# Optimization experiments

Hardware: AMD Instinct MI355X
Metric: run time of the kernel (lower is better)

## Reference

```python
import jax, jax.numpy as jnp
import numpy as np

SOS_TOKEN = 1
B, H, V, T = 64, 1024, 32000, 40
INPUT_SIZE = 4096


def setup_inputs() -> dict:
    key = jax.random.key(0)
    ks = jax.random.split(key, 12)
    s = 1.0 / np.sqrt(H)
    return {
        "output": jax.random.normal(ks[0], (B, INPUT_SIZE), jnp.float32),
        "h0": jax.random.normal(ks[1], (1, B, H), jnp.float32),
        "c0": jax.random.normal(ks[2], (1, B, H), jnp.float32),
        "target_outputs": jax.random.randint(ks[3], (B, T), 0, V, jnp.int64),
        "target_lengths": jnp.full((B,), T, jnp.int64),
        "embed": jax.random.normal(ks[4], (V, H), jnp.float32),
        "w_ih": jax.random.uniform(ks[5], (4 * H, H), jnp.float32, -s, s),
        "w_hh": jax.random.uniform(ks[6], (4 * H, H), jnp.float32, -s, s),
        "b_ih": jax.random.uniform(ks[7], (4 * H,), jnp.float32, -s, s),
        "b_hh": jax.random.uniform(ks[8], (4 * H,), jnp.float32, -s, s),
        "w_out": jax.random.uniform(ks[9], (V, H), jnp.float32, -s, s),
        "b_out": jax.random.uniform(ks[10], (V,), jnp.float32, -s, s),
    }


def _lstm_cell(x, h, c, w_ih, w_hh, b_ih, b_hh):
    # PyTorch LSTMCell math; gate order i, f, g, o
    gates = x @ w_ih.T + b_ih + h @ w_hh.T + b_hh  # [B, 4H]
    i, f, g, o = jnp.split(gates, 4, axis=-1)
    c2 = jax.nn.sigmoid(f) * c + jax.nn.sigmoid(i) * jnp.tanh(g)
    h2 = jax.nn.sigmoid(o) * jnp.tanh(c2)
    return h2, c2


def reference(output, h0, c0, target_outputs, target_lengths,
              embed, w_ih, w_hh, b_ih, b_hh, w_out, b_out):
    batch = output.shape[0]
    max_lens = int(jnp.max(target_lengths))
    h, c = h0[0], c0[0]  # num_layers=1 -> [B, H]

    # Initial symbol = SOS; initial dec_o = W(embed(SOS)) (no LSTM), as in torch code
    symbol0 = jnp.full((batch,), SOS_TOKEN, dtype=target_outputs.dtype)
    dec_o0 = embed[symbol0] @ w_out.T + b_out  # [B, V]

    def step(carry, _):
        symbol, dec_o, h, c = carry
        # emit current (symbol, dec_o), then decode next
        x = embed[symbol]  # [B, H]
        h2, c2 = _lstm_cell(x, h, c, w_ih, w_hh, b_ih, b_hh)
        dec2 = h2 @ w_out.T + b_out  # [B, V]
        sym2 = jnp.argmax(dec2, axis=-1).astype(symbol.dtype)  # greedy topk(1)
        return (sym2, dec2, h2, c2), (symbol, dec_o)
    (_, _, _, _), (symbols, decs) = jax.lax.scan(
        step, (symbol0, dec_o0, h, c), None, length=max_lens)

    decoder_outs = jnp.transpose(decs, (1, 0, 2))  # [B, T, V]
    symbol_outs = jnp.transpose(symbols, (1, 0))   # [B, T]
    return decoder_outs, symbol_outs
```

## Files before the change

kernel.cpp:

```cpp
#include <hip/hip_runtime.h>

#define Bdim 64
#define Hdim 1024
#define Vdim 32000
#define Tdim 40

typedef __bf16 bf16x8 __attribute__((ext_vector_type(8)));
typedef float  f32x4  __attribute__((ext_vector_type(4)));
static_assert(sizeof(bf16x8) == 16, "bf16x8 must be 16B");

__device__ __forceinline__ unsigned long long pack_key(float f, int v) {
    unsigned u = __float_as_uint(f);
    u = (u & 0x80000000u) ? ~u : (u | 0x80000000u);
    return ((unsigned long long)u << 32) | (unsigned long long)(0xFFFFFFFFu - (unsigned)v);
}

__device__ __forceinline__ void gll16(const void* g, void* l) {
    __builtin_amdgcn_global_load_lds(
        (const __attribute__((address_space(1))) void*)g,
        (__attribute__((address_space(3))) void*)l, 16, 0, 0);
}

__device__ __forceinline__ void bsplit3(float x, unsigned short& a, unsigned short& b,
                                        unsigned short& c) {
    __bf16 h = (__bf16)x;  float r  = x - (float)h;
    __bf16 m = (__bf16)r;  float r2 = r - (float)m;
    __bf16 l = (__bf16)r2;
    a = __builtin_bit_cast(unsigned short, h);
    b = __builtin_bit_cast(unsigned short, m);
    c = __builtin_bit_cast(unsigned short, l);
}

template<int NCH, bool ARGMAX, bool BIAS>
__device__ __forceinline__ void mm_core(
    const float* __restrict__ W,
    const unsigned short* __restrict__ Ah,
    const unsigned short* __restrict__ Am,
    const unsigned short* __restrict__ Al,
    int n0, const float* __restrict__ bias,
    float* __restrict__ out, size_t out_bstride,
    unsigned long long* __restrict__ slots)
{
    __shared__ __align__(16) unsigned char smem[2][20480];
    __shared__ unsigned long long red[4][4][16];

    const int tid  = threadIdx.x;
    const int lane = tid & 63;
    const int wid  = tid >> 6;

    f32x4 acc[4] = {};

    const unsigned char* Wb = (const unsigned char*)W;
    const unsigned char* Apb[3] = {(const unsigned char*)Ah, (const unsigned char*)Am,
                                   (const unsigned char*)Al};

    const int arws = tid >> 2, acs = tid & 3;
    const size_t asrc_off = (size_t)arws * 4096 + (size_t)(acs ^ ((arws >> 1) & 3)) * 16;

    auto stage = [&](int bufidx, int ch) {
        unsigned char* bb = smem[bufidx];
        const size_t kb4 = (size_t)ch * 128;
        const size_t kb2 = (size_t)ch * 64;
#pragma unroll
        for (int s = 0; s < 2; s++) {
            int gg = tid + 256 * s;
            int rw = gg >> 3, cc = gg & 7;
            int sg = cc ^ (rw & 7);
            gll16(Wb + (size_t)rw * 4096 + kb4 + (size_t)sg * 16,
                  bb + ((wid * 64 + 256 * s) << 4));
        }
#pragma unroll
        for (int pl = 0; pl < 3; pl++)
            gll16(Apb[pl] + asrc_off + kb2, bb + 8192 + pl * 4096 + (wid << 10));
    };

    stage(0, 0);
    __syncthreads();

    const int col  = lane & 15;
    const int kg   = lane >> 4;
    const int wrow = wid * 16 + col;
    const int wg0  = (2 * kg) ^ (wrow & 7);
    const int wg1  = (2 * kg + 1) ^ (wrow & 7);

#pragma unroll 2
    for (int ch = 0; ch < NCH; ch++) {
        if (ch + 1 < NCH) stage((ch + 1) & 1, ch + 1);
        unsigned char* base = smem[ch & 1];

        const unsigned char* Wr = base + wrow * 128;
        f32x4 w0 = *(const f32x4*)(Wr + (wg0 << 4));
        f32x4 w1 = *(const f32x4*)(Wr + (wg1 << 4));
        bf16x8 whi, wmid, wlo;
#pragma unroll
        for (int j = 0; j < 4; j++) {
            float x0 = w0[j], x1 = w1[j];
            __bf16 a0 = (__bf16)x0; float r0 = x0 - (float)a0;
            __bf16 b0 = (__bf16)r0; float q0 = r0 - (float)b0;
            whi[j] = a0; wmid[j] = b0; wlo[j] = (__bf16)q0;
            __bf16 a1 = (__bf16)x1; float r1 = x1 - (float)a1;
            __bf16 b1 = (__bf16)r1; float q1 = r1 - (float)b1;
            whi[4 + j] = a1; wmid[4 + j] = b1; wlo[4 + j] = (__bf16)q1;
        }
#pragma unroll
        for (int bt = 0; bt < 4; bt++) {
            const int arow = bt * 16 + col;
            const unsigned char* Ar = base + 8192 + arow * 64
                                    + ((kg ^ ((arow >> 1) & 3)) << 4);
            bf16x8 ahi = *(const bf16x8*)Ar;
            bf16x8 ami = *(const bf16x8*)(Ar + 4096);
            bf16x8 alo = *(const bf16x8*)(Ar + 8192);
            acc[bt] = __builtin_amdgcn_mfma_f32_16x16x32_bf16(whi,  ahi, acc[bt], 0, 0, 0);
            acc[bt] = __builtin_amdgcn_mfma_f32_16x16x32_bf16(whi,  ami, acc[bt], 0, 0, 0);
            acc[bt] = __builtin_amdgcn_mfma_f32_16x16x32_bf16(wmid, ahi, acc[bt], 0, 0, 0);
            acc[bt] = __builtin_amdgcn_mfma_f32_16x16x32_bf16(whi,  alo, acc[bt], 0, 0, 0);
            acc[bt] = __builtin_amdgcn_mfma_f32_16x16x32_bf16(wlo,  ahi, acc[bt], 0, 0, 0);
            acc[bt] = __builtin_amdgcn_mfma_f32_16x16x32_bf16(wmid, ami, acc[bt], 0, 0, 0);
        }
        __syncthreads();
    }

    const int ncol = n0 + wid * 16 + kg * 4;
    f32x4 bv = {};
    if (BIAS) bv = *(const f32x4*)(bias + ncol);

    unsigned long long bk[4];
#pragma unroll
    for (int bt = 0; bt < 4; bt++) {
        const int b = bt * 16 + col;
        float* op = out + (size_t)b * out_bstride + ncol;
        f32x4 vv;
        unsigned long long best = 0ull;
#pragma unroll
        for (int r = 0; r < 4; r++) {
            float val = acc[bt][r];
            if (BIAS) val += bv[r];
            vv[r] = val;
            if (ARGMAX) {
                unsigned long long key = pack_key(val, ncol + r);
                if (key > best) best = key;
            }
        }
        *(f32x4*)op = vv;
        bk[bt] = best;
    }

    if (ARGMAX) {
#pragma unroll
        for (int bt = 0; bt < 4; bt++) {
            unsigned long long k = bk[bt];
            unsigned long long o = __shfl_xor(k, 16, 64); if (o > k) k = o;
            o = __shfl_xor(k, 32, 64);                    if (o > k) k = o;
            if (lane < 16) red[wid][bt][lane] = k;
        }
        __syncthreads();
        if (tid < 64) {
            const int bt = tid >> 4, c = tid & 15;
            unsigned long long k = red[0][bt][c];
            if (red[1][bt][c] > k) k = red[1][bt][c];
            if (red[2][bt][c] > k) k = red[2][bt][c];
            if (red[3][bt][c] > k) k = red[3][bt][c];
            atomicMax(&slots[bt * 16 + c], k);
        }
    }
}

template<bool AM>
__global__ __launch_bounds__(256, 2) void k_logits(
    const float* __restrict__ w_out,
    const unsigned short* __restrict__ ah, const unsigned short* __restrict__ am,
    const unsigned short* __restrict__ al,
    const float* __restrict__ b_out, float* __restrict__ out,
    unsigned long long* __restrict__ slots)
{
    const int vb = blockIdx.x * 64;
    mm_core<32, AM, true>(w_out + (size_t)vb * Hdim, ah, am, al, vb, b_out,
                          out, (size_t)Tdim * Vdim, slots);
}

__global__ __launch_bounds__(256, 2) void k_gates(
    const float* __restrict__ w_ih, const float* __restrict__ w_hh,
    const unsigned short* __restrict__ xh_hi, const unsigned short* __restrict__ xh_mid,
    const unsigned short* __restrict__ xh_lo, float* __restrict__ gp)
{
    const int nb = blockIdx.x * 64;
    const int y = blockIdx.y, z = blockIdx.z;
    const float* W = (y ? w_hh : w_ih) + (size_t)nb * Hdim + z * 256;
    const int ao = y * 1024 + z * 256;
    mm_core<8, false, false>(W, xh_hi + ao, xh_mid + ao, xh_lo + ao, nb, nullptr,
                             gp + (size_t)(y * 4 + z) * (Bdim * 4096), 4096, nullptr);
}

__global__ void k_cell(const float* __restrict__ gp, const float* __restrict__ b_ih,
                       const float* __restrict__ b_hh, float* __restrict__ cbuf,
                       unsigned short* __restrict__ xh_hi, unsigned short* __restrict__ xh_mid,
                       unsigned short* __restrict__ xh_lo,
                       unsigned long long* __restrict__ slots)
{
    const int idx = blockIdx.x * 256 + threadIdx.x;
    const int b = idx >> 10, k = idx & 1023;
    const size_t S = (size_t)Bdim * 4096;
    const size_t base = (size_t)b * 4096;
    float g[4];
#pragma unroll
    for (int q = 0; q < 4; q++) {
        size_t o = base + q * 1024 + k;
        float s = gp[o];
#pragma unroll
        for (int i = 1; i < 8; i++) s += gp[i * S + o];
        g[q] = s + b_ih[q * 1024 + k] + b_hh[q * 1024 + k];
    }
    float si = 1.f / (1.f + expf(-g[0]));
    float sf = 1.f / (1.f + expf(-g[1]));
    float so = 1.f / (1.f + expf(-g[3]));
    float c  = cbuf[idx];
    float c2 = sf * c + si * tanhf(g[2]);
    float h2 = so * tanhf(c2);
    cbuf[idx] = c2;
    const size_t o = (size_t)b * 2048 + 1024 + k;
    unsigned short hs, ms, ls;
    bsplit3(h2, hs, ms, ls);
    xh_hi[o] = hs; xh_mid[o] = ms; xh_lo[o] = ls;
    if (idx < 64) slots[idx] = 0ull;
}

__global__ void k_symgather(const unsigned long long* __restrict__ slots,
                            const float* __restrict__ embed,
                            unsigned short* __restrict__ xh_hi,
                            unsigned short* __restrict__ xh_mid,
                            unsigned short* __restrict__ xh_lo,
                            float* __restrict__ sym_out, int t)
{
    __shared__ int s_sym;
    const int b = blockIdx.x, tid = threadIdx.x;
    if (tid == 0) {
        unsigned long long key = slots[b];
        int v = (int)(0xFFFFFFFFu - (unsigned)(key & 0xFFFFFFFFull));
        s_sym = v;
        sym_out[b * Tdim + t] = (float)v;
    }
    __syncthreads();
    const int v = s_sym;
    float4 e = *(const float4*)(embed + (size_t)v * Hdim + tid * 4);
    ushort4 hi, mi, lo;
    bsplit3(e.x, hi.x, mi.x, lo.x);
    bsplit3(e.y, hi.y, mi.y, lo.y);
    bsplit3(e.z, hi.z, mi.z, lo.z);
    bsplit3(e.w, hi.w, mi.w, lo.w);
    const size_t o = (size_t)b * 2048 + tid * 4;
    *(ushort4*)(xh_hi + o) = hi;
    *(ushort4*)(xh_mid + o) = mi;
    *(ushort4*)(xh_lo + o) = lo;
}

__global__ void k_init(const float* __restrict__ embed, const float* __restrict__ h0,
                       const float* __restrict__ c0,
                       unsigned short* __restrict__ xh_hi, unsigned short* __restrict__ xh_mid,
                       unsigned short* __restrict__ xh_lo,
                       float* __restrict__ cbuf, float* __restrict__ sym_out)
{
    const int b = blockIdx.x, tid = threadIdx.x;
    if (tid == 0) sym_out[b * Tdim] = 1.0f;
    const size_t xo = (size_t)b * 2048 + tid * 4;
    ushort4 hi, mi, lo;

    float4 e = *(const float4*)(embed + Hdim + tid * 4);
    bsplit3(e.x, hi.x, mi.x, lo.x);
    bsplit3(e.y, hi.y, mi.y, lo.y);
    bsplit3(e.z, hi.z, mi.z, lo.z);
    bsplit3(e.w, hi.w, mi.w, lo.w);
    *(ushort4*)(xh_hi + xo) = hi; *(ushort4*)(xh_mid + xo) = mi; *(ushort4*)(xh_lo + xo) = lo;

    float4 h = *(const float4*)(h0 + (size_t)b * Hdim + tid * 4);
    bsplit3(h.x, hi.x, mi.x, lo.x);
    bsplit3(h.y, hi.y, mi.y, lo.y);
    bsplit3(h.z, hi.z, mi.z, lo.z);
    bsplit3(h.w, hi.w, mi.w, lo.w);
    *(ushort4*)(xh_hi + xo + 1024) = hi;
    *(ushort4*)(xh_mid + xo + 1024) = mi;
    *(ushort4*)(xh_lo + xo + 1024) = lo;

    float4 c = *(const float4*)(c0 + (size_t)b * Hdim + tid * 4);
    *(float4*)(cbuf + (size_t)b * Hdim + tid * 4) = c;
}

extern "C" void kernel_launch(void* const* d_in, const int* in_sizes, int n_in,
                              void* d_out, int out_size, void* d_ws, size_t ws_size,
                              hipStream_t stream)
{
    const float* h0    = (const float*)d_in[1];
    const float* c0    = (const float*)d_in[2];
    const float* embed = (const float*)d_in[5];
    const float* w_ih  = (const float*)d_in[6];
    const float* w_hh  = (const float*)d_in[7];
    const float* b_ih  = (const float*)d_in[8];
    const float* b_hh  = (const float*)d_in[9];
    const float* w_out = (const float*)d_in[10];
    const float* b_out = (const float*)d_in[11];

    float* out = (float*)d_out;
    float* sym_out = out + (size_t)Bdim * Tdim * Vdim;

    unsigned short* xh_hi  = (unsigned short*)d_ws;
    unsigned short* xh_mid = xh_hi + (size_t)Bdim * 2048;
    unsigned short* xh_lo  = xh_mid + (size_t)Bdim * 2048;
    float* cbuf = (float*)(xh_lo + (size_t)Bdim * 2048);
    float* gp   = cbuf + (size_t)Bdim * Hdim;
    unsigned long long* slots = (unsigned long long*)(gp + 8ull * Bdim * 4096);

    k_init<<<Bdim, 256, 0, stream>>>(embed, h0, c0, xh_hi, xh_mid, xh_lo, cbuf, sym_out);

    k_logits<false><<<Vdim / 64, 256, 0, stream>>>(w_out, xh_hi, xh_mid, xh_lo,
                                                   b_out, out, slots);

    for (int t = 0; t < Tdim - 1; t++) {
        k_gates<<<dim3(64, 2, 4), 256, 0, stream>>>(w_ih, w_hh, xh_hi, xh_mid, xh_lo, gp);
        k_cell<<<Bdim * Hdim / 256, 256, 0, stream>>>(gp, b_ih, b_hh, cbuf,
                                                      xh_hi, xh_mid, xh_lo, slots);
        k_logits<true><<<Vdim / 64, 256, 0, stream>>>(w_out,
                                                      xh_hi + 1024, xh_mid + 1024, xh_lo + 1024,
                                                      b_out, out + (size_t)(t + 1) * Vdim, slots);
        k_symgather<<<Bdim, 256, 0, stream>>>(slots, embed, xh_hi, xh_mid, xh_lo,
                                              sym_out, t + 1);
    }
}
```

Baseline: 2.714 ms.

## Fuse symbol gather into gates GEMM and widen logits blocks to 128 columns

Removes the separate symbol-gather kernel: the x-half of the gates GEMM now decodes the argmax slot, gathers the embedding row directly from global memory and splits it into bf16 planes while staging into LDS. The logits kernel is widened to 8 waves covering 128 vocab columns per block (250 blocks, 512 threads), so the shared activation tiles are loaded once for twice as many output columns. The workspace is split into separate h and x planes, and a final tiny kernel writes the last symbol. This saves one launch per step and some A-tile traffic, but the gather path performs synchronous loads and conversion inside the pipelined stage, and the larger logits blocks change occupancy.

```diff
diff --git a/kernel.cpp b/kernel.cpp
--- a/kernel.cpp
+++ b/kernel.cpp
@@ -7,6 +7,7 @@
 
 typedef __bf16 bf16x8 __attribute__((ext_vector_type(8)));
 typedef float  f32x4  __attribute__((ext_vector_type(4)));
+typedef unsigned short u16x8 __attribute__((ext_vector_type(8)));
 static_assert(sizeof(bf16x8) == 16, "bf16x8 must be 16B");
 
 __device__ __forceinline__ unsigned long long pack_key(float f, int v) {
@@ -15,34 +16,53 @@
     return ((unsigned long long)u << 32) | (unsigned long long)(0xFFFFFFFFu - (unsigned)v);
 }
 
+__device__ __forceinline__ int decode_key(unsigned long long key) {
+    return (int)(0xFFFFFFFFu - (unsigned)(key & 0xFFFFFFFFull));
+}
+
 __device__ __forceinline__ void gll16(const void* g, void* l) {
     __builtin_amdgcn_global_load_lds(
         (const __attribute__((address_space(1))) void*)g,
         (__attribute__((address_space(3))) void*)l, 16, 0, 0);
 }
 
-__device__ __forceinline__ void bsplit3(float x, unsigned short& a, unsigned short& b,
-                                        unsigned short& c) {
+struct BSplit { unsigned short h, m, l; };
+
+__device__ __forceinline__ BSplit bsplit3v(float x) {
     __bf16 h = (__bf16)x;  float r  = x - (float)h;
     __bf16 m = (__bf16)r;  float r2 = r - (float)m;
     __bf16 l = (__bf16)r2;
-    a = __builtin_bit_cast(unsigned short, h);
-    b = __builtin_bit_cast(unsigned short, m);
-    c = __builtin_bit_cast(unsigned short, l);
-}
-
-template<int NCH, bool ARGMAX, bool BIAS>
+    BSplit s;
+    s.h = __builtin_bit_cast(unsigned short, h);
+    s.m = __builtin_bit_cast(unsigned short, m);
+    s.l = __builtin_bit_cast(unsigned short, l);
+    return s;
+}
+
+__device__ __forceinline__ void bsplit3(float x, unsigned short& a, unsigned short& b,
+                                        unsigned short& c) {
+    BSplit s = bsplit3v(x);
+    a = s.h; b = s.m; c = s.l;
+}
+
+template<int NW, int NCH, bool ARGMAX, bool BIAS, bool GATHER>
 __device__ __forceinline__ void mm_core(
+    unsigned char* sm,
+    unsigned long long (*red)[4][16],
     const float* __restrict__ W,
     const unsigned short* __restrict__ Ah,
     const unsigned short* __restrict__ Am,
     const unsigned short* __restrict__ Al,
+    const float* __restrict__ Gsrc,
+    const unsigned long long* __restrict__ slots_in, int tstep,
+    float* __restrict__ sym_dst,
     int n0, const float* __restrict__ bias,
     float* __restrict__ out, size_t out_bstride,
-    unsigned long long* __restrict__ slots)
-{
-    __shared__ __align__(16) unsigned char smem[2][20480];
-    __shared__ unsigned long long red[4][4][16];
+    unsigned long long* __restrict__ slots_out)
+{
+    constexpr int NT     = NW * 64;
+    constexpr int WBYTES = NW * 2048;
+    constexpr int BUFSZ  = WBYTES + 12288;
 
     const int tid  = threadIdx.x;
     const int lane = tid & 63;
@@ -54,24 +74,63 @@
     const unsigned char* Apb[3] = {(const unsigned char*)Ah, (const unsigned char*)Am,
                                    (const unsigned char*)Al};
 
-    const int arws = tid >> 2, acs = tid & 3;
-    const size_t asrc_off = (size_t)arws * 4096 + (size_t)(acs ^ ((arws >> 1) & 3)) * 16;
+    const int ar = tid >> 2, as = tid & 3;
+    const int aswz = as ^ ((ar >> 1) & 3);
+    const size_t asrc_off = (size_t)ar * 2048 + (size_t)aswz * 16;
+    const size_t aldst    = (size_t)ar * 64 + (size_t)aswz * 16;
+
+    const float* grow = nullptr;
+    if constexpr (GATHER) {
+        if (tid < 256) {
+            int symv = 1;
+            if (tstep > 0) {
+                unsigned long long key = slots_in[ar];
+                symv = decode_key(key);
+                if (sym_dst != nullptr && as == 0)
+                    sym_dst[ar * Tdim + tstep] = (float)symv;
+            }
+            grow = Gsrc + (size_t)symv * 1024 + as * 8;
+        }
+    }
 
     auto stage = [&](int bufidx, int ch) {
-        unsigned char* bb = smem[bufidx];
+        unsigned char* bb = sm + bufidx * BUFSZ;
         const size_t kb4 = (size_t)ch * 128;
-        const size_t kb2 = (size_t)ch * 64;
 #pragma unroll
         for (int s = 0; s < 2; s++) {
-            int gg = tid + 256 * s;
+            int gg = tid + NT * s;
             int rw = gg >> 3, cc = gg & 7;
             int sg = cc ^ (rw & 7);
             gll16(Wb + (size_t)rw * 4096 + kb4 + (size_t)sg * 16,
-                  bb + ((wid * 64 + 256 * s) << 4));
-        }
-#pragma unroll
-        for (int pl = 0; pl < 3; pl++)
-            gll16(Apb[pl] + asrc_off + kb2, bb + 8192 + pl * 4096 + (wid << 10));
+                  bb + ((wid * 64 + NT * s) << 4));
+        }
+        if constexpr (GATHER) {
+            if (tid < 256) {
+                const float* p = grow + ch * 32;
+                float4 f0 = *(const float4*)(p);
+                float4 f1 = *(const float4*)(p + 4);
+                u16x8 vh, vm, vl;
+                BSplit s0 = bsplit3v(f0.x); vh[0] = s0.h; vm[0] = s0.m; vl[0] = s0.l;
+                BSplit s1 = bsplit3v(f0.y); vh[1] = s1.h; vm[1] = s1.m; vl[1] = s1.l;
+                BSplit s2 = bsplit3v(f0.z); vh[2] = s2.h; vm[2] = s2.m; vl[2] = s2.l;
+                BSplit s3 = bsplit3v(f0.w); vh[3] = s3.h; vm[3] = s3.m; vl[3] = s3.l;
+                BSplit s4 = bsplit3v(f1.x); vh[4] = s4.h; vm[4] = s4.m; vl[4] = s4.l;
+                BSplit s5 = bsplit3v(f1.y); vh[5] = s5.h; vm[5] = s5.m; vl[5] = s5.l;
+                BSplit s6 = bsplit3v(f1.z); vh[6] = s6.h; vm[6] = s6.m; vl[6] = s6.l;
+                BSplit s7 = bsplit3v(f1.w); vh[7] = s7.h; vm[7] = s7.m; vl[7] = s7.l;
+                *(u16x8*)(bb + WBYTES + aldst)        = vh;
+                *(u16x8*)(bb + WBYTES + 4096 + aldst) = vm;
+                *(u16x8*)(bb + WBYTES + 8192 + aldst) = vl;
+            }
+        } else {
+            if (tid < 256) {
+                const size_t kb2 = (size_t)ch * 64;
+#pragma unroll
+                for (int pl = 0; pl < 3; pl++)
+                    gll16(Apb[pl] + asrc_off + kb2,
+                          bb + WBYTES + pl * 4096 + (wid << 10));
+            }
+        }
     };
 
     stage(0, 0);
@@ -86,7 +145,7 @@
 #pragma unroll 2
     for (int ch = 0; ch < NCH; ch++) {
         if (ch + 1 < NCH) stage((ch + 1) & 1, ch + 1);
-        unsigned char* base = smem[ch & 1];
+        unsigned char* base = sm + (ch & 1) * BUFSZ;
 
         const unsigned char* Wr = base + wrow * 128;
         f32x4 w0 = *(const f32x4*)(Wr + (wg0 << 4));
@@ -105,7 +164,7 @@
 #pragma unroll
         for (int bt = 0; bt < 4; bt++) {
             const int arow = bt * 16 + col;
-            const unsigned char* Ar = base + 8192 + arow * 64
+            const unsigned char* Ar = base + WBYTES + arow * 64
                                     + ((kg ^ ((arow >> 1) & 3)) << 4);
             bf16x8 ahi = *(const bf16x8*)Ar;
             bf16x8 ami = *(const bf16x8*)(Ar + 4096);
@@ -145,7 +204,7 @@
         bk[bt] = best;
     }
 
-    if (ARGMAX) {
+    if constexpr (ARGMAX) {
 #pragma unroll
         for (int bt = 0; bt < 4; bt++) {
             unsigned long long k = bk[bt];
@@ -157,44 +216,56 @@
         if (tid < 64) {
             const int bt = tid >> 4, c = tid & 15;
             unsigned long long k = red[0][bt][c];
-            if (red[1][bt][c] > k) k = red[1][bt][c];
-            if (red[2][bt][c] > k) k = red[2][bt][c];
-            if (red[3][bt][c] > k) k = red[3][bt][c];
-            atomicMax(&slots[bt * 16 + c], k);
+#pragma unroll
+            for (int w = 1; w < NW; w++)
+                if (red[w][bt][c] > k) k = red[w][bt][c];
+            atomicMax(&slots_out[bt * 16 + c], k);
         }
     }
 }
 
 template<bool AM>
-__global__ __launch_bounds__(256, 2) void k_logits(
+__global__ __launch_bounds__(512, 1) void k_logits(
     const float* __restrict__ w_out,
     const unsigned short* __restrict__ ah, const unsigned short* __restrict__ am,
     const unsigned short* __restrict__ al,
     const float* __restrict__ b_out, float* __restrict__ out,
     unsigned long long* __restrict__ slots)
 {
-    const int vb = blockIdx.x * 64;
-    mm_core<32, AM, true>(w_out + (size_t)vb * Hdim, ah, am, al, vb, b_out,
-                          out, (size_t)Tdim * Vdim, slots);
+    __shared__ __align__(16) unsigned char smem[2][28672];
+    __shared__ unsigned long long red[8][4][16];
+    const int vb = blockIdx.x * 128;
+    mm_core<8, 32, AM, true, false>(&smem[0][0], red,
+        w_out + (size_t)vb * Hdim, ah, am, al, nullptr, nullptr, 0, nullptr,
+        vb, b_out, out, (size_t)Tdim * Vdim, slots);
 }
 
 __global__ __launch_bounds__(256, 2) void k_gates(
     const float* __restrict__ w_ih, const float* __restrict__ w_hh,
-    const unsigned short* __restrict__ xh_hi, const unsigned short* __restrict__ xh_mid,
-    const unsigned short* __restrict__ xh_lo, float* __restrict__ gp)
-{
-    const int nb = blockIdx.x * 64;
-    const int y = blockIdx.y, z = blockIdx.z;
-    const float* W = (y ? w_hh : w_ih) + (size_t)nb * Hdim + z * 256;
-    const int ao = y * 1024 + z * 256;
-    mm_core<8, false, false>(W, xh_hi + ao, xh_mid + ao, xh_lo + ao, nb, nullptr,
-                             gp + (size_t)(y * 4 + z) * (Bdim * 4096), 4096, nullptr);
+    const unsigned short* __restrict__ hh, const unsigned short* __restrict__ hm,
+    const unsigned short* __restrict__ hl,
+    const float* __restrict__ embed, unsigned long long* __restrict__ slots,
+    int t, float* __restrict__ sym_out, float* __restrict__ gp)
+{
+    __shared__ __align__(16) unsigned char smem[2][20480];
+    const int nbi = blockIdx.x, y = blockIdx.y, z = blockIdx.z;
+    const float* W = (y ? w_hh : w_ih) + (size_t)nbi * 65536 + z * 256;
+    float* gout = gp + (size_t)(y * 4 + z) * (Bdim * 4096);
+    if (y)
+        mm_core<4, 8, false, false, false>(&smem[0][0], nullptr, W,
+            hh + z * 256, hm + z * 256, hl + z * 256, nullptr, nullptr, t, nullptr,
+            nbi * 64, nullptr, gout, 4096, nullptr);
+    else
+        mm_core<4, 8, false, false, true>(&smem[0][0], nullptr, W,
+            nullptr, nullptr, nullptr, embed + z * 256, slots, t,
+            ((nbi == 0 && z == 0) ? sym_out : nullptr),
+            nbi * 64, nullptr, gout, 4096, nullptr);
 }
 
 __global__ void k_cell(const float* __restrict__ gp, const float* __restrict__ b_ih,
                        const float* __restrict__ b_hh, float* __restrict__ cbuf,
-                       unsigned short* __restrict__ xh_hi, unsigned short* __restrict__ xh_mid,
-                       unsigned short* __restrict__ xh_lo,
+                       unsigned short* __restrict__ hh, unsigned short* __restrict__ hm,
+                       unsigned short* __restrict__ hl,
                        unsigned long long* __restrict__ slots)
 {
     const int idx = blockIdx.x * 256 + threadIdx.x;
@@ -217,71 +288,50 @@
     float c2 = sf * c + si * tanhf(g[2]);
     float h2 = so * tanhf(c2);
     cbuf[idx] = c2;
-    const size_t o = (size_t)b * 2048 + 1024 + k;
     unsigned short hs, ms, ls;
     bsplit3(h2, hs, ms, ls);
-    xh_hi[o] = hs; xh_mid[o] = ms; xh_lo[o] = ls;
+    const size_t o = (size_t)b * 1024 + k;
+    hh[o] = hs; hm[o] = ms; hl[o] = ls;
     if (idx < 64) slots[idx] = 0ull;
-}
-
-__global__ void k_symgather(const unsigned long long* __restrict__ slots,
-                            const float* __restrict__ embed,
-                            unsigned short* __restrict__ xh_hi,
-                            unsigned short* __restrict__ xh_mid,
-                            unsigned short* __restrict__ xh_lo,
-                            float* __restrict__ sym_out, int t)
-{
-    __shared__ int s_sym;
-    const int b = blockIdx.x, tid = threadIdx.x;
-    if (tid == 0) {
-        unsigned long long key = slots[b];
-        int v = (int)(0xFFFFFFFFu - (unsigned)(key & 0xFFFFFFFFull));
-        s_sym = v;
-        sym_out[b * Tdim + t] = (float)v;
-    }
-    __syncthreads();
-    const int v = s_sym;
-    float4 e = *(const float4*)(embed + (size_t)v * Hdim + tid * 4);
-    ushort4 hi, mi, lo;
-    bsplit3(e.x, hi.x, mi.x, lo.x);
-    bsplit3(e.y, hi.y, mi.y, lo.y);
-    bsplit3(e.z, hi.z, mi.z, lo.z);
-    bsplit3(e.w, hi.w, mi.w, lo.w);
-    const size_t o = (size_t)b * 2048 + tid * 4;
-    *(ushort4*)(xh_hi + o) = hi;
-    *(ushort4*)(xh_mid + o) = mi;
-    *(ushort4*)(xh_lo + o) = lo;
 }
 
 __global__ void k_init(const float* __restrict__ embed, const float* __restrict__ h0,
                        const float* __restrict__ c0,
-                       unsigned short* __restrict__ xh_hi, unsigned short* __restrict__ xh_mid,
-                       unsigned short* __restrict__ xh_lo,
-                       float* __restrict__ cbuf, float* __restrict__ sym_out)
-{
-    const int b = blockIdx.x, tid = threadIdx.x;
-    if (tid == 0) sym_out[b * Tdim] = 1.0f;
-    const size_t xo = (size_t)b * 2048 + tid * 4;
-    ushort4 hi, mi, lo;
-
-    float4 e = *(const float4*)(embed + Hdim + tid * 4);
-    bsplit3(e.x, hi.x, mi.x, lo.x);
-    bsplit3(e.y, hi.y, mi.y, lo.y);
-    bsplit3(e.z, hi.z, mi.z, lo.z);
-    bsplit3(e.w, hi.w, mi.w, lo.w);
-    *(ushort4*)(xh_hi + xo) = hi; *(ushort4*)(xh_mid + xo) = mi; *(ushort4*)(xh_lo + xo) = lo;
-
-    float4 h = *(const float4*)(h0 + (size_t)b * Hdim + tid * 4);
-    bsplit3(h.x, hi.x, mi.x, lo.x);
-    bsplit3(h.y, hi.y, mi.y, lo.y);
-    bsplit3(h.z, hi.z, mi.z, lo.z);
-    bsplit3(h.w, hi.w, mi.w, lo.w);
-    *(ushort4*)(xh_hi + xo + 1024) = hi;
-    *(ushort4*)(xh_mid + xo + 1024) = mi;
-    *(ushort4*)(xh_lo + xo + 1024) = lo;
-
-    float4 c = *(const float4*)(c0 + (size_t)b * Hdim + tid * 4);
-    *(float4*)(cbuf + (size_t)b * Hdim + tid * 4) = c;
+                       unsigned short* __restrict__ xsh, unsigned short* __restrict__ xsm,
+                       unsigned short* __restrict__ xsl,
+                       unsigned short* __restrict__ hh, unsigned short* __restrict__ hm,
+                       unsigned short* __restrict__ hl,
+                       float* __restrict__ cbuf, float* __restrict__ sym_out,
+                       unsigned long long* __restrict__ slots)
+{
+    const int b = blockIdx.x, t4 = threadIdx.x * 4;
+    if (threadIdx.x == 0) { sym_out[b * Tdim] = 1.0f; slots[b] = 0ull; }
+    const size_t o = (size_t)b * 1024 + t4;
+    ushort4 hi4, mi4, lo4;
+
+    float4 e = *(const float4*)(embed + 1024 + t4);
+    bsplit3(e.x, hi4.x, mi4.x, lo4.x);
+    bsplit3(e.y, hi4.y, mi4.y, lo4.y);
+    bsplit3(e.z, hi4.z, mi4.z, lo4.z);
+    bsplit3(e.w, hi4.w, mi4.w, lo4.w);
+    *(ushort4*)(xsh + o) = hi4; *(ushort4*)(xsm + o) = mi4; *(ushort4*)(xsl + o) = lo4;
+
+    float4 hv = *(const float4*)(h0 + (size_t)b * 1024 + t4);
+    bsplit3(hv.x, hi4.x, mi4.x, lo4.x);
+    bsplit3(hv.y, hi4.y, mi4.y, lo4.y);
+    bsplit3(hv.z, hi4.z, mi4.z, lo4.z);
+    bsplit3(hv.w, hi4.w, mi4.w, lo4.w);
+    *(ushort4*)(hh + o) = hi4; *(ushort4*)(hm + o) = mi4; *(ushort4*)(hl + o) = lo4;
+
+    float4 cv = *(const float4*)(c0 + (size_t)b * 1024 + t4);
+    *(float4*)(cbuf + (size_t)b * 1024 + t4) = cv;
+}
+
+__global__ void k_symfinal(const unsigned long long* __restrict__ slots,
+                           float* __restrict__ sym_out)
+{
+    const int b = threadIdx.x;
+    sym_out[b * Tdim + (Tdim - 1)] = (float)decode_key(slots[b]);
 }
 
 extern "C" void kernel_launch(void* const* d_in, const int* in_sizes, int n_in,
@@ -301,26 +351,30 @@
     float* out = (float*)d_out;
     float* sym_out = out + (size_t)Bdim * Tdim * Vdim;
 
-    unsigned short* xh_hi  = (unsigned short*)d_ws;
-    unsigned short* xh_mid = xh_hi + (size_t)Bdim * 2048;
-    unsigned short* xh_lo  = xh_mid + (size_t)Bdim * 2048;
-    float* cbuf = (float*)(xh_lo + (size_t)Bdim * 2048);
+    unsigned short* hh  = (unsigned short*)d_ws;
+    unsigned short* hm  = hh + (size_t)Bdim * 1024;
+    unsigned short* hl  = hm + (size_t)Bdim * 1024;
+    unsigned short* xsh = hl + (size_t)Bdim * 1024;
+    unsigned short* xsm = xsh + (size_t)Bdim * 1024;
+    unsigned short* xsl = xsm + (size_t)Bdim * 1024;
+    float* cbuf = (float*)(xsl + (size_t)Bdim * 1024);
     float* gp   = cbuf + (size_t)Bdim * Hdim;
     unsigned long long* slots = (unsigned long long*)(gp + 8ull * Bdim * 4096);
 
-    k_init<<<Bdim, 256, 0, stream>>>(embed, h0, c0, xh_hi, xh_mid, xh_lo, cbuf, sym_out);
-
-    k_logits<false><<<Vdim / 64, 256, 0, stream>>>(w_out, xh_hi, xh_mid, xh_lo,
-                                                   b_out, out, slots);
+    k_init<<<Bdim, 256, 0, stream>>>(embed, h0, c0, xsh, xsm, xsl,
+                                     hh, hm, hl, cbuf, sym_out, slots);
+
+    k_logits<false><<<Vdim / 128, 512, 0, stream>>>(w_out, xsh, xsm, xsl,
+                                                    b_out, out, slots);
 
     for (int t = 0; t < Tdim - 1; t++) {
-        k_gates<<<dim3(64, 2, 4), 256, 0, stream>>>(w_ih, w_hh, xh_hi, xh_mid, xh_lo, gp);
+        k_gates<<<dim3(64, 2, 4), 256, 0, stream>>>(w_ih, w_hh, hh, hm, hl,
+                                                    embed, slots, t, sym_out, gp);
         k_cell<<<Bdim * Hdim / 256, 256, 0, stream>>>(gp, b_ih, b_hh, cbuf,
-                                                      xh_hi, xh_mid, xh_lo, slots);
-        k_logits<true><<<Vdim / 64, 256, 0, stream>>>(w_out,
-                                                      xh_hi + 1024, xh_mid + 1024, xh_lo + 1024,
-                                                      b_out, out + (size_t)(t + 1) * Vdim, slots);
-        k_symgather<<<Bdim, 256, 0, stream>>>(slots, embed, xh_hi, xh_mid, xh_lo,
-                                              sym_out, t + 1);
-    }
-}
+                                                      hh, hm, hl, slots);
+        k_logits<true><<<Vdim / 128, 512, 0, stream>>>(w_out, hh, hm, hl,
+                                                       b_out, out + (size_t)(t + 1) * Vdim,
+                                                       slots);
+    }
+    k_symfinal<<<1, 64, 0, stream>>>(slots, sym_out);
+}
```

Result: faster. 2.606 ms (-4.0%).
